# Performance work log

Measured on AMD Instinct MI355X. Metric: run time of the kernel, lower is better.

The kernel has to match this reference:

```python
import jax, jax.numpy as jnp
import numpy as np
from jax import lax

B, S, I, H, O = 64, 512, 512, 1024, 2


def setup_inputs() -> dict:
    key = jax.random.key(0)
    ks = jax.random.split(key, 16)
    sc = 0.02
    def w(k, shape):
        return jax.random.normal(k, shape, dtype=jnp.float32) * sc
    inp = {
        "x": jax.random.normal(ks[0], (B, S, I), dtype=jnp.float32),
        # layer 0 GRU gates: Linear(I+H, H)
        "Wr0": w(ks[1], (H, I + H)), "br0": jnp.zeros((H,), jnp.float32),
        "Wz0": w(ks[2], (H, I + H)), "bz0": jnp.zeros((H,), jnp.float32),
        "Wc0": w(ks[3], (H, I + H)), "bc0": jnp.zeros((H,), jnp.float32),
        # layer 1 GRU gates: Linear(H+H, H)
        "Wr1": w(ks[4], (H, 2 * H)), "br1": jnp.zeros((H,), jnp.float32),
        "Wz1": w(ks[5], (H, 2 * H)), "bz1": jnp.zeros((H,), jnp.float32),
        "Wc1": w(ks[6], (H, 2 * H)), "bc1": jnp.zeros((H,), jnp.float32),
        "Wreg": w(ks[7], (O, H)), "breg": jnp.zeros((O,), jnp.float32),
    }
    return inp


def _gru_cell(h, xin, Wr, br, Wz, bz, Wc, bc):
    # Faithful to source GRUCell: note h*z + (1-z)*can (inverted vs standard GRU).
    xh = jnp.concatenate([xin, h], axis=1)
    r = jax.nn.sigmoid(xh @ Wr.T + br)
    z = jax.nn.sigmoid(xh @ Wz.T + bz)
    can = jnp.tanh(jnp.concatenate([xin, h * r], axis=1) @ Wc.T + bc)
    return h * z + (1.0 - z) * can


def reference(x, Wr0, br0, Wz0, bz0, Wc0, bc0, Wr1, br1, Wz1, bz1, Wc1, bc1, Wreg, breg):
    b = x.shape[0]
    hdim = Wr0.shape[0]
    h0_init = jnp.zeros((b, hdim), x.dtype)
    h1_init = jnp.zeros((b, hdim), x.dtype)

    def step(carry, xt):
        h0, h1 = carry
        h0 = _gru_cell(h0, xt, Wr0, br0, Wz0, bz0, Wc0, bc0)
        h1 = _gru_cell(h1, h0, Wr1, br1, Wz1, bz1, Wc1, bc1)
        return (h0, h1), None

    xs = jnp.swapaxes(x, 0, 1)  # [S, B, I]
    (h0, h1), _ = lax.scan(step, (h0_init, h1_init), xs)
    return h1 @ Wreg.T + breg
```

## Files before the change

kernel.cpp:

```cpp
#include <hip/hip_runtime.h>


typedef _Float16 f16;
typedef f16  f16x8 __attribute__((ext_vector_type(8)));
typedef float f32x4 __attribute__((ext_vector_type(4)));
typedef unsigned long long u64;

#define NB   64
#define SEQ  512
#define IDIM 512
#define HDIM 1024
#define NBH  (NB*HDIM)

#define OFF_H0   0u
#define OFF_H1   262144u
#define OFF_H0R  524288u
#define OFF_H1R  655360u
#define OFF_BAR  786432u
#define OFF_W16  790528u
#define W16_L0_ELEMS 4718592u

#define SMEM_BYTES 37888

__device__ __forceinline__ float sigf(float x){ return 1.0f/(1.0f+__expf(-x)); }
__device__ __forceinline__ float tanh_fast(float x){ float e=__expf(2.0f*x); return 1.0f - 2.0f/(e+1.0f); }

__device__ __forceinline__ f16x8 cload16(const f16* p){
  f16x8 r;
  asm volatile("global_load_dwordx4 %0, %1, off sc0 sc1" : "=v"(r) : "v"(p));
  return r;
}
__device__ __forceinline__ void cstore8(f16* p, u64 v){
  asm volatile("global_store_dwordx2 %0, %1, off sc0 sc1" :: "v"(p), "v"(v) : "memory");
}

__device__ __forceinline__ f16x8 load_x_frag(const float* p){
  f32x4 v0 = *(const f32x4*)p;
  f32x4 v1 = *(const f32x4*)(p+4);
  f16x8 r;
  r[0]=(f16)v0[0]; r[1]=(f16)v0[1]; r[2]=(f16)v0[2]; r[3]=(f16)v0[3];
  r[4]=(f16)v1[0]; r[5]=(f16)v1[1]; r[6]=(f16)v1[2]; r[7]=(f16)v1[3];
  return r;
}

__device__ __forceinline__ void group_barrier(char* gb, unsigned& lgen){
  asm volatile("s_waitcnt vmcnt(0) lgkmcnt(0)" ::: "memory");
  __syncthreads();
  if (threadIdx.x == 0){
    unsigned* cnt = (unsigned*)gb;
    unsigned* gen = (unsigned*)(gb + 256);
    const unsigned tgt = lgen + 1u;
    unsigned old = __hip_atomic_fetch_add(cnt, 1u, __ATOMIC_RELAXED, __HIP_MEMORY_SCOPE_AGENT);
    if (old == tgt*64u - 1u){
      __hip_atomic_store(gen, tgt, __ATOMIC_RELAXED, __HIP_MEMORY_SCOPE_AGENT);
    }
    while (__hip_atomic_load(gen, __ATOMIC_RELAXED, __HIP_MEMORY_SCOPE_AGENT) < tgt){
      __builtin_amdgcn_s_sleep(2);
    }
    lgen = tgt;
  }
  __syncthreads();
}

template<int LAYER>
__device__ void run_rnn(int g, int n32, const float* x,
    const float* brp, const float* bzp, const float* bcp,
    char* ws, char* smem, char* gb){
  constexpr int K   = (LAYER==0) ? 1536 : 2048;
  constexpr int NKS = K/32;
  constexpr int KW  = NKS/8;
  const int tid  = threadIdx.x;
  const int lane = tid & 63;
  const int kg   = tid >> 6;
  const int quad = lane >> 4;
  const int qo   = quad*8;
  const int m_base = g*16;
  const int n_base = n32*32;
  const int arow   = m_base + (lane & 15);

  f32x4* red = (f32x4*)smem;
  float* zst = (float*)(smem + 32768);
  f16*   hst = (f16*)  (smem + 34816);
  float* hf  = (float*)(smem + 35840);

  hf[tid & 511] = 0.f;
  __syncthreads();

  f16* h0m = (f16*)(ws + OFF_H0);
  f16* h1m = (f16*)(ws + OFF_H1);
  f16* h0r = (f16*)(ws + OFF_H0R);
  f16* h1r = (f16*)(ws + OFF_H1R);
  f16* hrbuf = (LAYER==0)? h0r : h1r;
  f16* hown  = (LAYER==0)? h0m : h1m;
  const char* w16L = ws + OFF_W16 + (LAYER ? (size_t)W16_L0_ELEMS*2 : 0);

  const size_t lo = (size_t)lane*16;
  const int nt0 = n32*2, nt1 = n32*2 + 1;
  const char* bR0 = w16L + ((size_t)((0*64 + nt0)*NKS + kg*KW))*1024 + lo;
  const char* bR1 = w16L + ((size_t)((0*64 + nt1)*NKS + kg*KW))*1024 + lo;
  const char* bZ0 = w16L + ((size_t)((1*64 + nt0)*NKS + kg*KW))*1024 + lo;
  const char* bZ1 = w16L + ((size_t)((1*64 + nt1)*NKS + kg*KW))*1024 + lo;
  const char* bC0 = w16L + ((size_t)((2*64 + nt0)*NKS + kg*KW))*1024 + lo;
  const char* bC1 = w16L + ((size_t)((2*64 + nt1)*NKS + kg*KW))*1024 + lo;

  const int col_own = n_base + (kg & 1)*16 + (lane & 15);
  const float bRv = brp[col_own], bZv = bzp[col_own], bCv = bcp[col_own];

  unsigned lgen = 0;
  f16x8 fa[KW];

  for (int iter = 0; iter <= SEQ; ++iter){
    const int  t    = (LAYER==0) ? iter : (iter-1);
    const bool act  = (LAYER==0) ? (iter < SEQ) : (iter >= 1);
    const int  bufA = (iter & 1) ^ 1;

    if (act){
#pragma unroll
      for (int j=0;j<KW;++j){
        int ks = kg*KW + j;
        if (LAYER==0){
          if (ks < 16)
            fa[j] = load_x_frag(x + ((size_t)arow*SEQ + t)*IDIM + ks*32 + qo);
          else
            fa[j] = cload16(h0m + (size_t)bufA*NBH + (size_t)arow*HDIM + (ks-16)*32 + qo);
        } else {
          if (ks < 32)
            fa[j] = cload16(h0m + (size_t)bufA*NBH + (size_t)arow*HDIM + ks*32 + qo);
          else
            fa[j] = cload16(h1m + (size_t)(iter&1)*NBH + (size_t)arow*HDIM + (ks-32)*32 + qo);
        }
      }
      asm volatile("s_waitcnt vmcnt(0)" ::: "memory");
      f32x4 aR0{0,0,0,0}, aR1{0,0,0,0}, aZ0{0,0,0,0}, aZ1{0,0,0,0};
#pragma unroll
      for (int j=0;j<KW;++j){
        aR0 = __builtin_amdgcn_mfma_f32_16x16x32_f16(fa[j], *(const f16x8*)(bR0 + j*1024), aR0,0,0,0);
        aR1 = __builtin_amdgcn_mfma_f32_16x16x32_f16(fa[j], *(const f16x8*)(bR1 + j*1024), aR1,0,0,0);
        aZ0 = __builtin_amdgcn_mfma_f32_16x16x32_f16(fa[j], *(const f16x8*)(bZ0 + j*1024), aZ0,0,0,0);
        aZ1 = __builtin_amdgcn_mfma_f32_16x16x32_f16(fa[j], *(const f16x8*)(bZ1 + j*1024), aZ1,0,0,0);
      }
      red[(0*8+kg)*64+lane] = aR0;  red[(1*8+kg)*64+lane] = aR1;
      red[(2*8+kg)*64+lane] = aZ0;  red[(3*8+kg)*64+lane] = aZ1;
    }
    __syncthreads();
    if (act && kg < 4){
      f32x4 s = red[(kg*8+0)*64+lane];
#pragma unroll
      for (int k2=1;k2<8;++k2) s += red[(kg*8+k2)*64+lane];
      const int coll = (kg&1)*16 + (lane&15);
#pragma unroll
      for (int i=0;i<4;++i){
        int rowl = quad*4 + i;
        if (kg < 2){
          float r = sigf(s[i] + bRv);
          hst[rowl*32 + coll] = (f16)(hf[rowl*32+coll] * r);
        } else {
          zst[rowl*32 + coll] = sigf(s[i] + bZv);
        }
      }
    }
    __syncthreads();
    if (act && tid < 128){
      int rowl = tid>>3, c8 = (tid&7)*4;
      u64 v = *(const u64*)(hst + rowl*32 + c8);
      cstore8(hrbuf + (size_t)(m_base+rowl)*HDIM + n_base + c8, v);
    }
    group_barrier(gb, lgen);

    if (act){
#pragma unroll
      for (int j=0;j<KW;++j){
        int ks = kg*KW + j;
        if (LAYER==0){
          if (ks >= 16)
            fa[j] = cload16(h0r + (size_t)arow*HDIM + (ks-16)*32 + qo);
        } else {
          if (ks >= 32)
            fa[j] = cload16(h1r + (size_t)arow*HDIM + (ks-32)*32 + qo);
        }
      }
      asm volatile("s_waitcnt vmcnt(0)" ::: "memory");
      f32x4 aC0{0,0,0,0}, aC1{0,0,0,0};
#pragma unroll
      for (int j=0;j<KW;++j){
        aC0 = __builtin_amdgcn_mfma_f32_16x16x32_f16(fa[j], *(const f16x8*)(bC0 + j*1024), aC0,0,0,0);
        aC1 = __builtin_amdgcn_mfma_f32_16x16x32_f16(fa[j], *(const f16x8*)(bC1 + j*1024), aC1,0,0,0);
      }
      red[(0*8+kg)*64+lane] = aC0;  red[(1*8+kg)*64+lane] = aC1;
    }
    __syncthreads();
    if (act && kg < 2){
      f32x4 s = red[(kg*8+0)*64+lane];
#pragma unroll
      for (int k2=1;k2<8;++k2) s += red[(kg*8+k2)*64+lane];
      const int coll = kg*16 + (lane&15);
#pragma unroll
      for (int i=0;i<4;++i){
        int rowl = quad*4 + i;
        float can = tanh_fast(s[i] + bCv);
        float z   = zst[rowl*32 + coll];
        float hnew = hf[rowl*32+coll]*z + (1.0f - z)*can;
        hf[rowl*32+coll]  = hnew;
        hst[rowl*32+coll] = (f16)hnew;
      }
    }
    __syncthreads();
    if (act && tid < 128){
      const int bufW = (LAYER==0) ? (iter&1) : ((iter&1)^1);
      int rowl = tid>>3, c8 = (tid&7)*4;
      u64 v = *(const u64*)(hst + rowl*32 + c8);
      cstore8(hown + (size_t)bufW*NBH + (size_t)(m_base+rowl)*HDIM + n_base + c8, v);
    }
    group_barrier(gb, lgen);
  }
}

__global__ void __launch_bounds__(512, 2)
rnn_kernel(const float* x,
           const float* br0, const float* bz0, const float* bc0,
           const float* br1, const float* bz1, const float* bc1,
           const float* Wreg, const float* breg,
           float* out, char* ws){
  extern __shared__ char smem[];
  const int b = blockIdx.x;
  const int xcd = b & 7, slot = b >> 3;
  const int g = slot & 3, phi = slot >> 2;
  const int p = phi*8 + xcd;
  const int layer = p >> 5, n32 = p & 31;
  char* gb = ws + OFF_BAR + (size_t)g*1024;

  if (layer==0) run_rnn<0>(g, n32, x, br0,bz0,bc0, ws, smem, gb);
  else          run_rnn<1>(g, n32, x, br1,bz1,bc1, ws, smem, gb);

  if (layer==1 && n32==0 && threadIdx.x < 32){
    int mrow = g*16 + ((int)threadIdx.x >> 1), o = threadIdx.x & 1;
    const f16* hp = (const f16*)(ws + OFF_H1) + (size_t)NBH + (size_t)mrow*HDIM;
    const float* wp = Wreg + (size_t)o*HDIM;
    float acc = 0.f;
#pragma unroll 4
    for (int k=0;k<HDIM;k+=4){
      u64 q = __hip_atomic_load((const u64*)(hp+k), __ATOMIC_RELAXED, __HIP_MEMORY_SCOPE_AGENT);
      union { u64 qq; f16 h[4]; } u; u.qq = q;
      acc += (float)u.h[0]*wp[k]   + (float)u.h[1]*wp[k+1]
           + (float)u.h[2]*wp[k+2] + (float)u.h[3]*wp[k+3];
    }
    out[mrow*2 + o] = acc + breg[o];
  }
}

__global__ void prep_w(const float* Wr0, const float* Wz0, const float* Wc0,
                       const float* Wr1, const float* Wz1, const float* Wc1,
                       f16* w16){
  size_t i = (size_t)blockIdx.x*256 + threadIdx.x;
  const bool l1 = (i >= (size_t)W16_L0_ELEMS);
  size_t j = l1 ? i - (size_t)W16_L0_ELEMS : i;
  const int K   = l1 ? 2048 : 1536;
  const int NKS = K >> 5;
  int e    = (int)(j & 7);
  int lane = (int)((j >> 3) & 63);
  size_t r = j >> 9;
  int ks   = (int)(r % (size_t)NKS);
  size_t gnt = r / (size_t)NKS;
  int nt   = (int)(gnt & 63);
  int gate = (int)(gnt >> 6);
  int n = nt*16 + (lane & 15);
  int k = ks*32 + ((lane >> 4) << 3) + e;
  const float* W = l1 ? (gate==0 ? Wr1 : gate==1 ? Wz1 : Wc1)
                      : (gate==0 ? Wr0 : gate==1 ? Wz0 : Wc0);
  w16[i] = (f16)W[(size_t)n*K + k];
}

extern "C" void kernel_launch(void* const* d_in, const int* in_sizes, int n_in,
                              void* d_out, int out_size, void* d_ws, size_t ws_size,
                              hipStream_t stream){
  const float* x    = (const float*)d_in[0];
  const float* Wr0  = (const float*)d_in[1];
  const float* br0  = (const float*)d_in[2];
  const float* Wz0  = (const float*)d_in[3];
  const float* bz0  = (const float*)d_in[4];
  const float* Wc0  = (const float*)d_in[5];
  const float* bc0  = (const float*)d_in[6];
  const float* Wr1  = (const float*)d_in[7];
  const float* br1  = (const float*)d_in[8];
  const float* Wz1  = (const float*)d_in[9];
  const float* bz1  = (const float*)d_in[10];
  const float* Wc1  = (const float*)d_in[11];
  const float* bc1  = (const float*)d_in[12];
  const float* Wreg = (const float*)d_in[13];
  const float* breg = (const float*)d_in[14];
  float* out = (float*)d_out;
  char*  ws  = (char*)d_ws;

  hipMemsetAsync(ws, 0, OFF_W16, stream);

  prep_w<<<43008, 256, 0, stream>>>(Wr0, Wz0, Wc0, Wr1, Wz1, Wc1,
                                    (f16*)(ws + OFF_W16));

  hipFuncSetAttribute((const void*)rnn_kernel,
                      hipFuncAttributeMaxDynamicSharedMemorySize, 160*1024);

  void* args[] = { (void*)&x,
                   (void*)&br0, (void*)&bz0, (void*)&bc0,
                   (void*)&br1, (void*)&bz1, (void*)&bc1,
                   (void*)&Wreg, (void*)&breg,
                   (void*)&out, (void*)&ws };
  hipLaunchCooperativeKernel((const void*)rnn_kernel, dim3(256), dim3(512),
                             args, (unsigned)SMEM_BYTES, stream);
}
```

Baseline: 6.321 ms.

## Replace group atomic barrier with per-block flags and overlap Z/C work with sync

Replaces the counter+generation group barrier with per-block flag arrays. Each block publishes its step count and then polls only the flags it depends on: its own layer's 32 blocks for the r*h exchange, and all 64 blocks for the hidden-state exchange. The Z-gate GEMM and the x-part of the candidate GEMM now run between publishing r*h and waiting for it, so that compute hides barrier latency. The x fragments for layer 0 are prefetched a step ahead, and stores are widened to 16 bytes. This adds spinning by up to 64 threads with no sleep, and the flag protocol relies on relaxed atomics for ordering.

```diff
diff --git a/kernel.cpp b/kernel.cpp
--- a/kernel.cpp
+++ b/kernel.cpp
@@ -16,11 +16,14 @@
 #define OFF_H1   262144u
 #define OFF_H0R  524288u
 #define OFF_H1R  655360u
-#define OFF_BAR  786432u
+#define OFF_FLA  786432u
+#define OFF_FLB  787456u
 #define OFF_W16  790528u
 #define W16_L0_ELEMS 4718592u
 
 #define SMEM_BYTES 37888
+
+#define MFMA16 __builtin_amdgcn_mfma_f32_16x16x32_f16
 
 __device__ __forceinline__ float sigf(float x){ return 1.0f/(1.0f+__expf(-x)); }
 __device__ __forceinline__ float tanh_fast(float x){ float e=__expf(2.0f*x); return 1.0f - 2.0f/(e+1.0f); }
@@ -30,8 +33,8 @@
   asm volatile("global_load_dwordx4 %0, %1, off sc0 sc1" : "=v"(r) : "v"(p));
   return r;
 }
-__device__ __forceinline__ void cstore8(f16* p, u64 v){
-  asm volatile("global_store_dwordx2 %0, %1, off sc0 sc1" :: "v"(p), "v"(v) : "memory");
+__device__ __forceinline__ void cstore16(f16* p, f16x8 v){
+  asm volatile("global_store_dwordx4 %0, %1, off sc0 sc1" :: "v"(p), "v"(v) : "memory");
 }
 
 __device__ __forceinline__ f16x8 load_x_frag(const float* p){
@@ -43,32 +46,14 @@
   return r;
 }
 
-__device__ __forceinline__ void group_barrier(char* gb, unsigned& lgen){
-  asm volatile("s_waitcnt vmcnt(0) lgkmcnt(0)" ::: "memory");
-  __syncthreads();
-  if (threadIdx.x == 0){
-    unsigned* cnt = (unsigned*)gb;
-    unsigned* gen = (unsigned*)(gb + 256);
-    const unsigned tgt = lgen + 1u;
-    unsigned old = __hip_atomic_fetch_add(cnt, 1u, __ATOMIC_RELAXED, __HIP_MEMORY_SCOPE_AGENT);
-    if (old == tgt*64u - 1u){
-      __hip_atomic_store(gen, tgt, __ATOMIC_RELAXED, __HIP_MEMORY_SCOPE_AGENT);
-    }
-    while (__hip_atomic_load(gen, __ATOMIC_RELAXED, __HIP_MEMORY_SCOPE_AGENT) < tgt){
-      __builtin_amdgcn_s_sleep(2);
-    }
-    lgen = tgt;
-  }
-  __syncthreads();
-}
-
 template<int LAYER>
 __device__ void run_rnn(int g, int n32, const float* x,
     const float* brp, const float* bzp, const float* bcp,
-    char* ws, char* smem, char* gb){
+    char* ws, char* smem, unsigned* flA, unsigned* flB, int slotB){
   constexpr int K   = (LAYER==0) ? 1536 : 2048;
   constexpr int NKS = K/32;
   constexpr int KW  = NKS/8;
+  constexpr int XKS = (LAYER==0) ? 16 : 32;
   const int tid  = threadIdx.x;
   const int lane = tid & 63;
   const int kg   = tid >> 6;
@@ -88,10 +73,8 @@
 
   f16* h0m = (f16*)(ws + OFF_H0);
   f16* h1m = (f16*)(ws + OFF_H1);
-  f16* h0r = (f16*)(ws + OFF_H0R);
-  f16* h1r = (f16*)(ws + OFF_H1R);
-  f16* hrbuf = (LAYER==0)? h0r : h1r;
-  f16* hown  = (LAYER==0)? h0m : h1m;
+  f16* hrbuf = (LAYER==0) ? (f16*)(ws + OFF_H0R) : (f16*)(ws + OFF_H1R);
+  f16* hown  = (LAYER==0) ? h0m : h1m;
   const char* w16L = ws + OFF_W16 + (LAYER ? (size_t)W16_L0_ELEMS*2 : 0);
 
   const size_t lo = (size_t)lane*16;
@@ -106,22 +89,30 @@
   const int col_own = n_base + (kg & 1)*16 + (lane & 15);
   const float bRv = brp[col_own], bZv = bzp[col_own], bCv = bcp[col_own];
 
-  unsigned lgen = 0;
+  unsigned lgA = 0, lgB = 0;
   f16x8 fa[KW];
+  f16x8 xf[KW];
+
+  if (LAYER==0){
+#pragma unroll
+    for (int j=0;j<KW;++j){
+      int ks = kg*KW + j;
+      if (ks < XKS) xf[j] = load_x_frag(x + ((size_t)arow*SEQ + 0)*IDIM + ks*32 + qo);
+    }
+  }
 
   for (int iter = 0; iter <= SEQ; ++iter){
-    const int  t    = (LAYER==0) ? iter : (iter-1);
     const bool act  = (LAYER==0) ? (iter < SEQ) : (iter >= 1);
     const int  bufA = (iter & 1) ^ 1;
 
+    f32x4 aC0{0,0,0,0}, aC1{0,0,0,0};
+
     if (act){
 #pragma unroll
       for (int j=0;j<KW;++j){
         int ks = kg*KW + j;
         if (LAYER==0){
-          if (ks < 16)
-            fa[j] = load_x_frag(x + ((size_t)arow*SEQ + t)*IDIM + ks*32 + qo);
-          else
+          if (ks >= XKS)
             fa[j] = cload16(h0m + (size_t)bufA*NBH + (size_t)arow*HDIM + (ks-16)*32 + qo);
         } else {
           if (ks < 32)
@@ -130,88 +121,161 @@
             fa[j] = cload16(h1m + (size_t)(iter&1)*NBH + (size_t)arow*HDIM + (ks-32)*32 + qo);
         }
       }
+      f16x8 wA[KW], wB[KW];
+#pragma unroll
+      for (int j=0;j<KW;++j){
+        wA[j] = *(const f16x8*)(bR0 + j*1024);
+        wB[j] = *(const f16x8*)(bR1 + j*1024);
+      }
       asm volatile("s_waitcnt vmcnt(0)" ::: "memory");
-      f32x4 aR0{0,0,0,0}, aR1{0,0,0,0}, aZ0{0,0,0,0}, aZ1{0,0,0,0};
-#pragma unroll
-      for (int j=0;j<KW;++j){
-        aR0 = __builtin_amdgcn_mfma_f32_16x16x32_f16(fa[j], *(const f16x8*)(bR0 + j*1024), aR0,0,0,0);
-        aR1 = __builtin_amdgcn_mfma_f32_16x16x32_f16(fa[j], *(const f16x8*)(bR1 + j*1024), aR1,0,0,0);
-        aZ0 = __builtin_amdgcn_mfma_f32_16x16x32_f16(fa[j], *(const f16x8*)(bZ0 + j*1024), aZ0,0,0,0);
-        aZ1 = __builtin_amdgcn_mfma_f32_16x16x32_f16(fa[j], *(const f16x8*)(bZ1 + j*1024), aZ1,0,0,0);
-      }
-      red[(0*8+kg)*64+lane] = aR0;  red[(1*8+kg)*64+lane] = aR1;
-      red[(2*8+kg)*64+lane] = aZ0;  red[(3*8+kg)*64+lane] = aZ1;
-    }
-    __syncthreads();
-    if (act && kg < 4){
+      __builtin_amdgcn_sched_barrier(0);
+      f32x4 aR0{0,0,0,0}, aR1{0,0,0,0};
+#pragma unroll
+      for (int j=0;j<KW;++j){
+        int ks = kg*KW + j;
+        const f16x8 a = (LAYER==0 && ks < XKS) ? xf[j] : fa[j];
+        aR0 = MFMA16(a, wA[j], aR0, 0,0,0);
+        aR1 = MFMA16(a, wB[j], aR1, 0,0,0);
+      }
+      red[(0*8+kg)*64+lane] = aR0;
+      red[(1*8+kg)*64+lane] = aR1;
+    }
+    __syncthreads();
+    if (act && kg < 2){
       f32x4 s = red[(kg*8+0)*64+lane];
 #pragma unroll
       for (int k2=1;k2<8;++k2) s += red[(kg*8+k2)*64+lane];
-      const int coll = (kg&1)*16 + (lane&15);
+      const int coll = kg*16 + (lane & 15);
 #pragma unroll
       for (int i=0;i<4;++i){
         int rowl = quad*4 + i;
-        if (kg < 2){
-          float r = sigf(s[i] + bRv);
-          hst[rowl*32 + coll] = (f16)(hf[rowl*32+coll] * r);
-        } else {
-          zst[rowl*32 + coll] = sigf(s[i] + bZv);
+        float r = sigf(s[i] + bRv);
+        hst[rowl*32 + coll] = (f16)(hf[rowl*32 + coll] * r);
+      }
+    }
+    __syncthreads();
+    if (act && tid < 64){
+      int rowl = tid >> 2, c8 = (tid & 3)*8;
+      f16x8 v = *(const f16x8*)(hst + rowl*32 + c8);
+      cstore16(hrbuf + (size_t)(m_base+rowl)*HDIM + n_base + c8, v);
+    }
+    asm volatile("s_waitcnt vmcnt(0) lgkmcnt(0)" ::: "memory");
+    ++lgA;
+    if (tid == 0)
+      __hip_atomic_store(flA + n32, lgA, __ATOMIC_RELAXED, __HIP_MEMORY_SCOPE_AGENT);
+
+    if (act){
+      f16x8 wA[KW], wB[KW];
+#pragma unroll
+      for (int j=0;j<KW;++j){
+        wA[j] = *(const f16x8*)(bZ0 + j*1024);
+        wB[j] = *(const f16x8*)(bZ1 + j*1024);
+      }
+      f32x4 aZ0{0,0,0,0}, aZ1{0,0,0,0};
+#pragma unroll
+      for (int j=0;j<KW;++j){
+        int ks = kg*KW + j;
+        const f16x8 a = (LAYER==0 && ks < XKS) ? xf[j] : fa[j];
+        aZ0 = MFMA16(a, wA[j], aZ0, 0,0,0);
+        aZ1 = MFMA16(a, wB[j], aZ1, 0,0,0);
+      }
+      red[(2*8+kg)*64+lane] = aZ0;
+      red[(3*8+kg)*64+lane] = aZ1;
+#pragma unroll
+      for (int j=0;j<KW;++j){
+        int ks = kg*KW + j;
+        if (ks < XKS){
+          const f16x8 a = (LAYER==0) ? xf[j] : fa[j];
+          aC0 = MFMA16(a, *(const f16x8*)(bC0 + j*1024), aC0, 0,0,0);
+          aC1 = MFMA16(a, *(const f16x8*)(bC1 + j*1024), aC1, 0,0,0);
         }
       }
     }
     __syncthreads();
-    if (act && tid < 128){
-      int rowl = tid>>3, c8 = (tid&7)*4;
-      u64 v = *(const u64*)(hst + rowl*32 + c8);
-      cstore8(hrbuf + (size_t)(m_base+rowl)*HDIM + n_base + c8, v);
-    }
-    group_barrier(gb, lgen);
-
+    if (act && (kg == 2 || kg == 3)){
+      f32x4 s = red[(kg*8+0)*64+lane];
+#pragma unroll
+      for (int k2=1;k2<8;++k2) s += red[(kg*8+k2)*64+lane];
+      const int coll = (kg & 1)*16 + (lane & 15);
+#pragma unroll
+      for (int i=0;i<4;++i)
+        zst[(quad*4+i)*32 + coll] = sigf(s[i] + bZv);
+    }
+    if (tid < 32){
+      while (__hip_atomic_load(flA + tid, __ATOMIC_RELAXED, __HIP_MEMORY_SCOPE_AGENT) < lgA) {}
+    }
+    __syncthreads();
+
+    if (act && (kg+1)*KW > XKS){
+#pragma unroll
+      for (int j=0;j<KW;++j){
+        int ks = kg*KW + j;
+        if (ks >= XKS)
+          fa[j] = cload16(hrbuf + (size_t)arow*HDIM + (ks-XKS)*32 + qo);
+      }
+      f16x8 wA[KW], wB[KW];
+#pragma unroll
+      for (int j=0;j<KW;++j){
+        int ks = kg*KW + j;
+        if (ks >= XKS){
+          wA[j] = *(const f16x8*)(bC0 + j*1024);
+          wB[j] = *(const f16x8*)(bC1 + j*1024);
+        }
+      }
+      asm volatile("s_waitcnt vmcnt(0)" ::: "memory");
+      __builtin_amdgcn_sched_barrier(0);
+#pragma unroll
+      for (int j=0;j<KW;++j){
+        int ks = kg*KW + j;
+        if (ks >= XKS){
+          aC0 = MFMA16(fa[j], wA[j], aC0, 0,0,0);
+          aC1 = MFMA16(fa[j], wB[j], aC1, 0,0,0);
+        }
+      }
+    }
     if (act){
-#pragma unroll
-      for (int j=0;j<KW;++j){
-        int ks = kg*KW + j;
-        if (LAYER==0){
-          if (ks >= 16)
-            fa[j] = cload16(h0r + (size_t)arow*HDIM + (ks-16)*32 + qo);
-        } else {
-          if (ks >= 32)
-            fa[j] = cload16(h1r + (size_t)arow*HDIM + (ks-32)*32 + qo);
-        }
-      }
-      asm volatile("s_waitcnt vmcnt(0)" ::: "memory");
-      f32x4 aC0{0,0,0,0}, aC1{0,0,0,0};
-#pragma unroll
-      for (int j=0;j<KW;++j){
-        aC0 = __builtin_amdgcn_mfma_f32_16x16x32_f16(fa[j], *(const f16x8*)(bC0 + j*1024), aC0,0,0,0);
-        aC1 = __builtin_amdgcn_mfma_f32_16x16x32_f16(fa[j], *(const f16x8*)(bC1 + j*1024), aC1,0,0,0);
-      }
-      red[(0*8+kg)*64+lane] = aC0;  red[(1*8+kg)*64+lane] = aC1;
+      red[(0*8+kg)*64+lane] = aC0;
+      red[(1*8+kg)*64+lane] = aC1;
     }
     __syncthreads();
     if (act && kg < 2){
       f32x4 s = red[(kg*8+0)*64+lane];
 #pragma unroll
       for (int k2=1;k2<8;++k2) s += red[(kg*8+k2)*64+lane];
-      const int coll = kg*16 + (lane&15);
+      const int coll = kg*16 + (lane & 15);
 #pragma unroll
       for (int i=0;i<4;++i){
         int rowl = quad*4 + i;
         float can = tanh_fast(s[i] + bCv);
         float z   = zst[rowl*32 + coll];
-        float hnew = hf[rowl*32+coll]*z + (1.0f - z)*can;
-        hf[rowl*32+coll]  = hnew;
-        hst[rowl*32+coll] = (f16)hnew;
-      }
-    }
-    __syncthreads();
-    if (act && tid < 128){
+        float hnew = hf[rowl*32 + coll]*z + (1.0f - z)*can;
+        hf[rowl*32 + coll]  = hnew;
+        hst[rowl*32 + coll] = (f16)hnew;
+      }
+    }
+    __syncthreads();
+    if (act && tid < 64){
       const int bufW = (LAYER==0) ? (iter&1) : ((iter&1)^1);
-      int rowl = tid>>3, c8 = (tid&7)*4;
-      u64 v = *(const u64*)(hst + rowl*32 + c8);
-      cstore8(hown + (size_t)bufW*NBH + (size_t)(m_base+rowl)*HDIM + n_base + c8, v);
-    }
-    group_barrier(gb, lgen);
+      int rowl = tid >> 2, c8 = (tid & 3)*8;
+      f16x8 v = *(const f16x8*)(hst + rowl*32 + c8);
+      cstore16(hown + (size_t)bufW*NBH + (size_t)(m_base+rowl)*HDIM + n_base + c8, v);
+    }
+    asm volatile("s_waitcnt vmcnt(0) lgkmcnt(0)" ::: "memory");
+    ++lgB;
+    if (tid == 0)
+      __hip_atomic_store(flB + slotB, lgB, __ATOMIC_RELAXED, __HIP_MEMORY_SCOPE_AGENT);
+    if (LAYER==0 && iter+1 < SEQ){
+#pragma unroll
+      for (int j=0;j<KW;++j){
+        int ks = kg*KW + j;
+        if (ks < XKS)
+          xf[j] = load_x_frag(x + ((size_t)arow*SEQ + (iter+1))*IDIM + ks*32 + qo);
+      }
+    }
+    if (tid < 64){
+      while (__hip_atomic_load(flB + tid, __ATOMIC_RELAXED, __HIP_MEMORY_SCOPE_AGENT) < lgB) {}
+    }
+    __syncthreads();
   }
 }
 
@@ -227,20 +291,22 @@
   const int g = slot & 3, phi = slot >> 2;
   const int p = phi*8 + xcd;
   const int layer = p >> 5, n32 = p & 31;
-  char* gb = ws + OFF_BAR + (size_t)g*1024;
-
-  if (layer==0) run_rnn<0>(g, n32, x, br0,bz0,bc0, ws, smem, gb);
-  else          run_rnn<1>(g, n32, x, br1,bz1,bc1, ws, smem, gb);
+  unsigned* flA = (unsigned*)(ws + OFF_FLA) + (g*2 + layer)*32;
+  unsigned* flB = (unsigned*)(ws + OFF_FLB) + g*64;
+  const int slotB = layer*32 + n32;
+
+  if (layer==0) run_rnn<0>(g, n32, x, br0,bz0,bc0, ws, smem, flA, flB, slotB);
+  else          run_rnn<1>(g, n32, x, br1,bz1,bc1, ws, smem, flA, flB, slotB);
 
   if (layer==1 && n32==0 && threadIdx.x < 32){
     int mrow = g*16 + ((int)threadIdx.x >> 1), o = threadIdx.x & 1;
-    const f16* hp = (const f16*)(ws + OFF_H1) + (size_t)NBH + (size_t)mrow*HDIM;
+    const _Float16* hp = (const _Float16*)(ws + OFF_H1) + (size_t)NBH + (size_t)mrow*HDIM;
     const float* wp = Wreg + (size_t)o*HDIM;
     float acc = 0.f;
 #pragma unroll 4
     for (int k=0;k<HDIM;k+=4){
       u64 q = __hip_atomic_load((const u64*)(hp+k), __ATOMIC_RELAXED, __HIP_MEMORY_SCOPE_AGENT);
-      union { u64 qq; f16 h[4]; } u; u.qq = q;
+      union { u64 qq; _Float16 h[4]; } u; u.qq = q;
       acc += (float)u.h[0]*wp[k]   + (float)u.h[1]*wp[k+1]
            + (float)u.h[2]*wp[k+2] + (float)u.h[3]*wp[k+3];
     }
```

Measured after the change: 5.757 ms, median of 2. 1.1x faster.
